# Kernel tuning notes

Measured on AMD Instinct MI355X. Metric: run time of the kernel, lower is better.

The kernel has to match this reference:

```python
import jax, jax.numpy as jnp
import numpy as np


def _phi(x):
    # ELU(x) + 1 feature map (positive kernel feature map)
    return jax.nn.elu(x) + 1.0


def setup_inputs() -> dict:
    key = jax.random.key(0)
    k1, k2, k3 = jax.random.split(key, 3)
    B, S, E = 4, 4096, 1024
    inputs = jax.random.normal(k1, (B, S, E), dtype=jnp.float32)
    mask = jnp.ones((B, S), dtype=jnp.float32)
    w_qkv = jax.random.normal(k2, (3 * E, E), dtype=jnp.float32) * (E ** -0.5)
    b_qkv = jax.random.normal(k3, (3 * E,), dtype=jnp.float32) * 0.02
    return {"inputs": inputs, "mask": mask, "w_qkv": w_qkv, "b_qkv": b_qkv, "num_heads": 16}


def reference(inputs, mask, w_qkv, b_qkv, num_heads):
    B, S, E = inputs.shape
    H = num_heads
    D = E // H
    # qkv projection: torch Linear is x @ W.T + b
    qkv = inputs @ w_qkv.T + b_qkv                     # (B, S, 3E)
    qkv = qkv.reshape(B, S, 3, H, D)
    q = qkv[:, :, 0]                                   # (B, S, H, D)
    k = qkv[:, :, 1]
    v = qkv[:, :, 2]
    # key masking (float multiply, as in einsum 'bshd,bs->bshd')
    k = k * mask[:, :, None, None]
    kq = _phi(q)                                       # (B, S, H, D)
    kk = _phi(k)                                       # (B, S, H, D)
    # kv outer-product accumulation over sequence: (B, H, M, D)
    kv = jnp.einsum('bshd,bshm->bhmd', kk, v)
    # normalizer
    z = 1.0 / (jnp.einsum('bshd,bhd->bsh', kq, kk.sum(axis=1)) + 1e-6)
    # final contraction
    attn = jnp.einsum('bshd,bhmd,bsh->bshm', kq, kv, z)  # (B, S, H, D)
    attn = attn.reshape(B, S, E)
    # NOTE: original forward computes a projection but returns `attn` (dropout is
    # identity at inference), so projection is dead code and omitted here.
    return attn
```

## Files before the change

### kernel.cpp

```cpp
#include <hip/hip_runtime.h>

typedef unsigned short u16;
typedef short bf16x8 __attribute__((ext_vector_type(8)));
typedef float f32x4 __attribute__((ext_vector_type(4)));
typedef u16 u16x8 __attribute__((ext_vector_type(8)));
typedef u16 u16x4 __attribute__((ext_vector_type(4)));

#define B_ 4
#define S_ 4096
#define E_ 1024
#define H_ 16
#define D_ 64
#define M_ 16384
#define N_ 3072
#define K_ 1024

__device__ __forceinline__ u16 f2b(float f) {
    unsigned x = __builtin_bit_cast(unsigned, f);
    return (u16)((x + 0x7fffu + ((x >> 16) & 1u)) >> 16);
}
__device__ __forceinline__ float b2f(u16 u) {
    unsigned x = ((unsigned)u) << 16;
    return __builtin_bit_cast(float, x);
}
__device__ __forceinline__ float phi_f(float x) { return x > 0.f ? x + 1.f : __expf(x); }

__device__ __forceinline__ void gload16(const void* g, void* l) {
    __builtin_amdgcn_global_load_lds((const __attribute__((address_space(1))) void*)g,
                                     (__attribute__((address_space(3))) void*)l, 16, 0, 0);
}

#define MEMFENCE asm volatile("" ::: "memory")
#define BAR { MEMFENCE; __builtin_amdgcn_s_barrier(); MEMFENCE; }
#define LGKM0 { asm volatile("s_waitcnt lgkmcnt(0)" ::: "memory"); \
                __builtin_amdgcn_sched_barrier(0); }
#define VMCNT(n) asm volatile("s_waitcnt vmcnt(" #n ")" ::: "memory")

__global__ void cvt_bf16(const float* __restrict__ in, u16* __restrict__ out, int n8) {
    int stride = gridDim.x * blockDim.x;
    for (int i = blockIdx.x * blockDim.x + threadIdx.x; i < n8; i += stride) {
        const float4* p = (const float4*)(in + (size_t)i * 8);
        float4 a = p[0], b = p[1];
        u16x8 o;
        o[0] = f2b(a.x); o[1] = f2b(a.y); o[2] = f2b(a.z); o[3] = f2b(a.w);
        o[4] = f2b(b.x); o[5] = f2b(b.y); o[6] = f2b(b.z); o[7] = f2b(b.w);
        *(u16x8*)(out + (size_t)i * 8) = o;
    }
}


#define RD_A(BO, MI0) { _Pragma("unroll") for (int m_ = 0; m_ < 4; ++m_) { \
    av[m_][0] = *(const bf16x8*)(aB + (BO) + (MI0 + m_) * 2048 + pc0); \
    av[m_][1] = *(const bf16x8*)(aB + (BO) + (MI0 + m_) * 2048 + pc1); } }

#define RD_B01(BO) { _Pragma("unroll") for (int n_ = 0; n_ < 2; ++n_) { \
    b01[n_][0] = *(const bf16x8*)(bB + (BO) + n_ * 2048 + pc0); \
    b01[n_][1] = *(const bf16x8*)(bB + (BO) + n_ * 2048 + pc1); } }

#define RD_B23(BO) { _Pragma("unroll") for (int n_ = 0; n_ < 2; ++n_) { \
    b23[n_][0] = *(const bf16x8*)(bB + (BO) + (2 + n_) * 2048 + pc0); \
    b23[n_][1] = *(const bf16x8*)(bB + (BO) + (2 + n_) * 2048 + pc1); } }

#define ST_A(TT, HI, BO) { \
    gload16(gA + (size_t)((HI) * 64) * K_ + (TT) * 64, lds + (BO) + (HI) * 8192 + t16); \
    gload16(gA + (size_t)((HI) * 64 + 128) * K_ + (TT) * 64, lds + (BO) + 16384 + (HI) * 8192 + t16); }

#define ST_B(TT, PR, BO) { \
    gload16(gB + (size_t)((PR) * 128) * K_ + (TT) * 64, lds + (BO) + 32768 + (PR) * 16384 + t16); \
    gload16(gB + (size_t)((PR) * 128 + 64) * K_ + (TT) * 64, lds + (BO) + 32768 + (PR) * 16384 + 8192 + t16); }

#define MM16(MI0, NI0, BV) { __builtin_amdgcn_s_setprio(1); \
    _Pragma("unroll") for (int m_ = 0; m_ < 4; ++m_) \
    _Pragma("unroll") for (int n_ = 0; n_ < 2; ++n_) \
    _Pragma("unroll") for (int h_ = 0; h_ < 2; ++h_) \
        acc[(MI0) + m_][(NI0) + n_] = __builtin_amdgcn_mfma_f32_16x16x32_bf16( \
            av[m_][h_], BV[n_][h_], acc[(MI0) + m_][(NI0) + n_], 0, 0, 0); \
    __builtin_amdgcn_s_setprio(0); }

__device__ __forceinline__ void run_tile(
    const u16* gA, const u16* gB, char* lds, int t16,
    const char* aB, const char* bB, int pc0, int pc1, f32x4 (&acc)[8][4])
{
    bf16x8 av[4][2], b01[2][2], b23[2][2];
    ST_A(0, 0, 0); ST_B(0, 0, 0); ST_B(0, 1, 0); ST_A(0, 1, 0);
    ST_A(1, 0, 65536); ST_B(1, 0, 65536);
    VMCNT(4);
    __builtin_amdgcn_s_barrier();
    MEMFENCE;
#pragma unroll 1
    for (int kt = 0; kt < 16; kt += 2) {
        int tp2 = kt + 2 < 16 ? kt + 2 : 15;
        int tp3 = kt + 3 < 16 ? kt + 3 : 15;
        RD_A(0, 0); RD_B01(0); ST_A(kt + 1, 1, 65536); BAR; LGKM0; MM16(0, 0, b01);
        RD_B23(0);  ST_B(kt + 1, 1, 65536);            BAR; LGKM0; MM16(0, 2, b23);
        RD_A(0, 4); ST_A(tp2, 0, 0);                   BAR; LGKM0; MM16(4, 2, b23);
        ST_B(tp2, 0, 0); VMCNT(4);                     BAR; LGKM0; MM16(4, 0, b01);
        RD_A(65536, 0); RD_B01(65536); ST_A(tp2, 1, 0); BAR; LGKM0; MM16(0, 0, b01);
        RD_B23(65536);  ST_B(tp2, 1, 0);                BAR; LGKM0; MM16(0, 2, b23);
        RD_A(65536, 4); ST_A(tp3, 0, 65536);            BAR; LGKM0; MM16(4, 2, b23);
        ST_B(tp3, 0, 65536); VMCNT(4);                  BAR; LGKM0; MM16(4, 0, b01);
    }
    VMCNT(0);
    __builtin_amdgcn_s_barrier();
    MEMFENCE;
}

__global__ __launch_bounds__(512, 2) void gemm_fused(
    const u16* __restrict__ Abf, const u16* __restrict__ Wbf,
    const float* __restrict__ bias, const float* __restrict__ mask,
    u16* __restrict__ KQ, u16* VT,
    float* __restrict__ KVP, float* __restrict__ KSP)
{
    __shared__ __align__(16) char lds[131072];

    int wg  = blockIdx.x;
    int xcd = wg & 7, ii = wg >> 3;
    int tm  = xcd * 8 + (ii >> 2);
    int g   = ii & 3;
    int m0  = tm << 8;
    int b   = tm >> 4;
    int s0  = (tm & 15) << 8;

    int t = threadIdx.x;
    int l = t & 63, wid = t >> 6;
    int wr = wid >> 2, wc = wid & 3;
    int lg = l >> 4, lr = l & 15;

    int srow  = t >> 3;
    int scolE = ((t & 7) ^ (srow & 7)) << 3;
    int t16   = t * 16;

    const u16* gA = Abf + (size_t)(m0 + srow) * K_ + scolE;
    const char* aB = lds + (wr * 128 + lr) * 128;
    const char* bB = lds + 32768 + (wc * 64 + lr) * 128;
    int pc0 = (lg * 16) ^ ((lr & 7) << 4);
    int pc1 = pc0 ^ 64;

    {
        int n0 = 2048 + g * 256;
        const u16* gB = Wbf + (size_t)(n0 + srow) * K_ + scolE;
        f32x4 acc[8][4] = {};
        run_tile(gA, gB, lds, t16, aB, bB, pc0, pc1, acc);
        float bv[4];
#pragma unroll
        for (int ni = 0; ni < 4; ++ni) bv[ni] = bias[n0 + wc * 64 + ni * 16 + lr];
        int h = g * 4 + wc;
#pragma unroll
        for (int mi = 0; mi < 8; ++mi) {
            int sbase = s0 + wr * 128 + mi * 16 + lg * 4;
#pragma unroll
            for (int ni = 0; ni < 4; ++ni) {
                u16x4 o;
#pragma unroll
                for (int j = 0; j < 4; ++j) o[j] = f2b(acc[mi][ni][j] + bv[ni]);
                int d = ni * 16 + lr;
                *(u16x4*)(VT + ((size_t)((b * H_ + h) * D_ + d)) * S_ + sbase) = o;
            }
        }
    }

    {
        int n0 = 1024 + g * 256;
        const u16* gB = Wbf + (size_t)(n0 + srow) * K_ + scolE;
        f32x4 acc[8][4] = {};
        run_tile(gA, gB, lds, t16, aB, bB, pc0, pc1, acc);
        float bv[4];
#pragma unroll
        for (int ni = 0; ni < 4; ++ni) bv[ni] = bias[n0 + wc * 64 + ni * 16 + lr];
#pragma unroll
        for (int mi = 0; mi < 8; ++mi) {
            int sl0 = wr * 128 + mi * 16 + lg * 4;
            float mk[4];
#pragma unroll
            for (int j = 0; j < 4; ++j) mk[j] = mask[m0 + sl0 + j];
#pragma unroll
            for (int ni = 0; ni < 4; ++ni) {
                int d = ni * 16 + lr;
                u16x4 o;
#pragma unroll
                for (int j = 0; j < 4; ++j)
                    o[j] = f2b(phi_f((acc[mi][ni][j] + bv[ni]) * mk[j]));
                *(u16x4*)(lds + wc * 32768 + d * 512 + ((sl0 * 2) ^ ((d & 7) << 4))) = o;
            }
        }
    }
    __syncthreads();

    {
        int head = wid & 3, mh = wid >> 2;
        int bh = b * 16 + g * 4 + head;
        f32x4 akv[2][4] = {};
        const u16* vbase = VT + ((size_t)(bh * 64 + mh * 32 + lr)) * S_ + s0;
#pragma unroll
        for (int ks = 0; ks < 8; ++ks) {
            bf16x8 vf[2];
#pragma unroll
            for (int mi = 0; mi < 2; ++mi)
                vf[mi] = *(const bf16x8*)(vbase + (size_t)mi * 16 * S_ + ks * 32 + lg * 8);
#pragma unroll
            for (int ni = 0; ni < 4; ++ni) {
                int dd = ni * 16 + lr;
                bf16x8 kf = *(const bf16x8*)(lds + head * 32768 + dd * 512 +
                                             ((ks * 64 + lg * 16) ^ ((dd & 7) << 4)));
                akv[0][ni] = __builtin_amdgcn_mfma_f32_16x16x32_bf16(vf[0], kf, akv[0][ni], 0, 0, 0);
                akv[1][ni] = __builtin_amdgcn_mfma_f32_16x16x32_bf16(vf[1], kf, akv[1][ni], 0, 0, 0);
            }
        }
        float* kvp = KVP + ((size_t)(tm & 15) * 64 + bh) * 4096;
#pragma unroll
        for (int mi = 0; mi < 2; ++mi)
#pragma unroll
            for (int ni = 0; ni < 4; ++ni)
#pragma unroll
                for (int j = 0; j < 4; ++j)
                    kvp[(mh * 32 + mi * 16 + lg * 4 + j) * 64 + ni * 16 + lr] = akv[mi][ni][j];
        int hd = t >> 7, dd2 = (t >> 1) & 63, hf = t & 1;
        float ksm = 0.f;
#pragma unroll
        for (int i = 0; i < 16; ++i) {
            bf16x8 kk8 = *(const bf16x8*)(lds + hd * 32768 + dd2 * 512 +
                                          ((hf * 256 + i * 16) ^ ((dd2 & 7) << 4)));
#pragma unroll
            for (int e = 0; e < 8; ++e) ksm += b2f((u16)kk8[e]);
        }
        ksm += __shfl_xor(ksm, 1);
        if (!hf) KSP[(tm & 15) * 4096 + (b * 16 + g * 4 + hd) * 64 + dd2] = ksm;
    }
    __syncthreads();

    {
        int n0 = g * 256;
        const u16* gB = Wbf + (size_t)(n0 + srow) * K_ + scolE;
        f32x4 acc[8][4] = {};
        run_tile(gA, gB, lds, t16, aB, bB, pc0, pc1, acc);
        float bv[4];
#pragma unroll
        for (int ni = 0; ni < 4; ++ni) bv[ni] = bias[n0 + wc * 64 + ni * 16 + lr];
#pragma unroll
        for (int mi = 0; mi < 8; ++mi)
#pragma unroll
            for (int j = 0; j < 4; ++j) {
                int row = m0 + wr * 128 + mi * 16 + lg * 4 + j;
#pragma unroll
                for (int ni = 0; ni < 4; ++ni) {
                    int col = n0 + wc * 64 + ni * 16 + lr;
                    KQ[(size_t)row * E_ + col] = f2b(phi_f(acc[mi][ni][j] + bv[ni]));
                }
            }
    }
}

__global__ void reduce_kv(const float* __restrict__ KVP, const float* __restrict__ KSP,
                          float* __restrict__ KV, float* __restrict__ KSUM)
{
    int g = blockIdx.x * 256 + threadIdx.x;
#pragma unroll 1
    for (int i = g * 4; i < g * 4 + 4; ++i) {
        float s = 0.f;
#pragma unroll
        for (int c = 0; c < 16; ++c) s += KVP[(size_t)c * (64 * 4096) + i];
        KV[i] = s;
    }
    if (g < 4096) {
        float s = 0.f;
#pragma unroll
        for (int c = 0; c < 16; ++c) s += KSP[c * 4096 + g];
        KSUM[g] = s;
    }
}

__global__ __launch_bounds__(256) void attn_out(
    const u16* __restrict__ KQ, const float* __restrict__ KV,
    const float* __restrict__ KSUM, float* __restrict__ Out)
{
    __shared__ __align__(16) u16 kqs[16384];
    __shared__ __align__(16) u16 bsm[5120];
    __shared__ float den[256];
    int bh = blockIdx.x, ch = blockIdx.y;
    int b = bh >> 4, h = bh & 15;
    int t = threadIdx.x;
    int l = t & 63, w = t >> 6;
    int lg = l >> 4, lr = l & 15;
    size_t row0 = (size_t)b * S_ + ch * 256;
    int srow = t >> 3, scol = (t & 7) << 3;
#pragma unroll
    for (int i = 0; i < 8; ++i)
        gload16(KQ + (row0 + srow + i * 32) * E_ + h * 64 + scol, kqs + i * 2048 + t * 8);

    const float* kvg = KV + bh * 4096;
#pragma unroll
    for (int ii = 0; ii < 16; ii += 4) {
        float4 v = *(const float4*)(kvg + t * 16 + ii);
        u16x4 o; o[0] = f2b(v.x); o[1] = f2b(v.y); o[2] = f2b(v.z); o[3] = f2b(v.w);
        *(u16x4*)&bsm[t * 16 + ii] = o;
    }
    if (t < 64) bsm[4096 + t] = f2b(KSUM[bh * 64 + t]);
    for (int i = t; i < 960; i += 256) bsm[4160 + i] = 0;
    __syncthreads();

    f32x4 acc[4][5] = {};
#pragma unroll
    for (int kh = 0; kh < 2; ++kh) {
        int ko = kh * 32 + lg * 8;
        bf16x8 af[4];
#pragma unroll
        for (int mi = 0; mi < 4; ++mi)
            af[mi] = *(const bf16x8*)&kqs[(w * 64 + mi * 16 + lr) * 64 + ko];
#pragma unroll
        for (int ni = 0; ni < 5; ++ni) {
            bf16x8 bb = *(const bf16x8*)&bsm[(ni * 16 + lr) * 64 + ko];
#pragma unroll
            for (int mi = 0; mi < 4; ++mi)
                acc[mi][ni] = __builtin_amdgcn_mfma_f32_16x16x32_bf16(af[mi], bb, acc[mi][ni], 0, 0, 0);
        }
    }
    if (lr == 0) {
#pragma unroll
        for (int mi = 0; mi < 4; ++mi)
#pragma unroll
            for (int j = 0; j < 4; ++j)
                den[w * 64 + mi * 16 + lg * 4 + j] = acc[mi][4][j];
    }
    __syncthreads();
#pragma unroll
    for (int mi = 0; mi < 4; ++mi)
#pragma unroll
        for (int j = 0; j < 4; ++j) {
            int sl = w * 64 + mi * 16 + lg * 4 + j;
            float z = 1.f / (den[sl] + 1e-6f);
            float* op = Out + (row0 + sl) * E_ + h * 64;
#pragma unroll
            for (int ni = 0; ni < 4; ++ni)
                op[ni * 16 + lr] = acc[mi][ni][j] * z;
        }
}

extern "C" void kernel_launch(void* const* d_in, const int* in_sizes, int n_in,
                              void* d_out, int out_size, void* d_ws, size_t ws_size,
                              hipStream_t stream)
{
    const float* inputs = (const float*)d_in[0];
    const float* mask   = (const float*)d_in[1];
    const float* w_qkv  = (const float*)d_in[2];
    const float* b_qkv  = (const float*)d_in[3];

    u16* Abf = (u16*)d_ws;
    u16* Wbf = Abf + (size_t)M_ * K_;
    u16* KQ  = Wbf + (size_t)N_ * K_;
    float* KVP  = (float*)(KQ + (size_t)M_ * E_);
    float* KSP  = KVP + 16 * 64 * 4096;
    float* KV   = KSP + 16 * 4096;
    float* KSUM = KV + 64 * 4096;

    u16* VT = (u16*)d_out;

    cvt_bf16<<<2048, 256, 0, stream>>>(inputs, Abf, M_ * K_ / 8);
    cvt_bf16<<<768, 256, 0, stream>>>(w_qkv, Wbf, N_ * K_ / 8);
    gemm_fused<<<256, 512, 0, stream>>>(Abf, Wbf, b_qkv, mask, KQ, VT, KVP, KSP);
    reduce_kv<<<256, 256, 0, stream>>>(KVP, KSP, KV, KSUM);
    attn_out<<<dim3(64, 16), 256, 0, stream>>>(KQ, KV, KSUM, (float*)d_out);
}
```

Measured before the change: 156.2 us.

## Split Q projection into a second GEMM fused with attention output

The Q-projection GEMM moves out of the V/K kernel into a new kernel that runs it after the KV reduction and applies phi(Q)·KV plus the normalizer straight from registers via LDS. This removes the bf16 KQ intermediate round-trip through HBM and the separate attn_out kernel. The reduction now emits a pre-swizzled bf16 KV/ksum block in one step. In exchange, the K/V GEMM kernel loses its overlap with the Q tile, and the new kernel adds an LDS staging phase and extra barriers after the main GEMM.

Measured after the change: 187.4 us. +20.0%, slower.

```diff
diff --git a/kernel.cpp b/kernel.cpp
--- a/kernel.cpp
+++ b/kernel.cpp
@@ -105,11 +105,10 @@
     MEMFENCE;
 }
 
-__global__ __launch_bounds__(512, 2) void gemm_fused(
+__global__ __launch_bounds__(512, 2) void gemm_vk(
     const u16* __restrict__ Abf, const u16* __restrict__ Wbf,
     const float* __restrict__ bias, const float* __restrict__ mask,
-    u16* __restrict__ KQ, u16* VT,
-    float* __restrict__ KVP, float* __restrict__ KSP)
+    u16* VT, float* __restrict__ KVP, float* __restrict__ KSP)
 {
     __shared__ __align__(16) char lds[131072];
 
@@ -226,113 +225,140 @@
         ksm += __shfl_xor(ksm, 1);
         if (!hf) KSP[(tm & 15) * 4096 + (b * 16 + g * 4 + hd) * 64 + dd2] = ksm;
     }
+}
+
+__global__ void reduce_kvb(const float* __restrict__ KVP, const float* __restrict__ KSP,
+                           u16* __restrict__ KVB)
+{
+    int bh = blockIdx.x;
+    int t = threadIdx.x;
+    int d = t & 63, mg = t >> 6;
+#pragma unroll 1
+    for (int i = 0; i < 16; ++i) {
+        int m = mg * 16 + i;
+        float s = 0.f;
+#pragma unroll
+        for (int c = 0; c < 16; ++c)
+            s += KVP[((size_t)c * 64 + bh) * 4096 + m * 64 + d];
+        KVB[((size_t)bh * 80 + m) * 64 + (d ^ ((m & 7) << 3))] = f2b(s);
+    }
+    if (mg == 0) {
+        float s = 0.f;
+#pragma unroll
+        for (int c = 0; c < 16; ++c) s += KSP[c * 4096 + bh * 64 + d];
+        KVB[((size_t)bh * 80 + 64) * 64 + d] = f2b(s);
+    }
+    for (int m = 65 + mg; m < 80; m += 4)
+        KVB[((size_t)bh * 80 + m) * 64 + (d ^ ((m & 7) << 3))] = 0;
+}
+
+__global__ __launch_bounds__(512, 2) void gemm_qattn(
+    const u16* __restrict__ Abf, const u16* __restrict__ Wbf,
+    const float* __restrict__ bias, const u16* __restrict__ KVB,
+    float* __restrict__ Out)
+{
+    __shared__ __align__(16) char lds[131072];
+
+    int wg  = blockIdx.x;
+    int xcd = wg & 7, ii = wg >> 3;
+    int tm  = xcd * 8 + (ii >> 2);
+    int g   = ii & 3;
+    int m0  = tm << 8;
+    int b   = tm >> 4;
+
+    int t = threadIdx.x;
+    int l = t & 63, wid = t >> 6;
+    int wr = wid >> 2, wc = wid & 3;
+    int lg = l >> 4, lr = l & 15;
+
+    int srow  = t >> 3;
+    int scolE = ((t & 7) ^ (srow & 7)) << 3;
+    int t16   = t * 16;
+
+    const u16* gA = Abf + (size_t)(m0 + srow) * K_ + scolE;
+    const char* aB = lds + (wr * 128 + lr) * 128;
+    const char* bB = lds + 32768 + (wc * 64 + lr) * 128;
+    int pc0 = (lg * 16) ^ ((lr & 7) << 4);
+    int pc1 = pc0 ^ 64;
+
+    int n0 = g * 256;
+    const u16* gB = Wbf + (size_t)(n0 + srow) * K_ + scolE;
+    f32x4 acc[8][4] = {};
+    run_tile(gA, gB, lds, t16, aB, bB, pc0, pc1, acc);
+
+    {
+        const u16* kvbg = KVB + (size_t)(b * 16 + g * 4) * 80 * 64;
+#pragma unroll
+        for (int i = 0; i < 5; ++i)
+            gload16(kvbg + i * 4096 + t * 8, lds + i * 8192 + t16);
+    }
+    float bv[4];
+#pragma unroll
+    for (int ni = 0; ni < 4; ++ni) bv[ni] = bias[n0 + wc * 64 + ni * 16 + lr];
+#pragma unroll
+    for (int mi = 0; mi < 8; ++mi)
+#pragma unroll
+        for (int ni = 0; ni < 4; ++ni)
+#pragma unroll
+            for (int j = 0; j < 4; ++j)
+                acc[mi][ni][j] = phi_f(acc[mi][ni][j] + bv[ni]);
+    VMCNT(0);
     __syncthreads();
 
-    {
-        int n0 = g * 256;
-        const u16* gB = Wbf + (size_t)(n0 + srow) * K_ + scolE;
-        f32x4 acc[8][4] = {};
-        run_tile(gA, gB, lds, t16, aB, bB, pc0, pc1, acc);
-        float bv[4];
-#pragma unroll
-        for (int ni = 0; ni < 4; ++ni) bv[ni] = bias[n0 + wc * 64 + ni * 16 + lr];
-#pragma unroll
-        for (int mi = 0; mi < 8; ++mi)
+#pragma unroll
+    for (int r = 0; r < 2; ++r) {
+        __syncthreads();
+        if (wr == r) {
+#pragma unroll
+            for (int mi = 0; mi < 8; ++mi)
+#pragma unroll
+                for (int j = 0; j < 4; ++j) {
+                    int sl = mi * 16 + lg * 4 + j;
+                    int swz = (sl & 7) << 4;
+#pragma unroll
+                    for (int ni = 0; ni < 4; ++ni) {
+                        int d2 = (ni * 16 + lr) * 2;
+                        *(u16*)(lds + 40960 + sl * 512 + wc * 128 + (d2 ^ swz)) =
+                            f2b(acc[mi][ni][j]);
+                    }
+                }
+        }
+        __syncthreads();
+
+        f32x4 a2[4][5] = {};
+#pragma unroll
+        for (int kh = 0; kh < 2; ++kh) {
+            bf16x8 af[4];
+#pragma unroll
+            for (int mi2 = 0; mi2 < 4; ++mi2) {
+                int sl = wr * 64 + mi2 * 16 + lr;
+                af[mi2] = *(const bf16x8*)(lds + 40960 + sl * 512 + wc * 128 +
+                                           ((kh * 64 + lg * 16) ^ ((sl & 7) << 4)));
+            }
+#pragma unroll
+            for (int ni2 = 0; ni2 < 5; ++ni2) {
+                int m = ni2 * 16 + lr;
+                bf16x8 bf_ = *(const bf16x8*)(lds + wc * 10240 + m * 128 +
+                                              ((kh * 64 + lg * 16) ^ ((m & 7) << 4)));
+#pragma unroll
+                for (int mi2 = 0; mi2 < 4; ++mi2)
+                    a2[mi2][ni2] = __builtin_amdgcn_mfma_f32_16x16x32_bf16(
+                        af[mi2], bf_, a2[mi2][ni2], 0, 0, 0);
+            }
+        }
+#pragma unroll
+        for (int mi2 = 0; mi2 < 4; ++mi2)
 #pragma unroll
             for (int j = 0; j < 4; ++j) {
-                int row = m0 + wr * 128 + mi * 16 + lg * 4 + j;
-#pragma unroll
-                for (int ni = 0; ni < 4; ++ni) {
-                    int col = n0 + wc * 64 + ni * 16 + lr;
-                    KQ[(size_t)row * E_ + col] = f2b(phi_f(acc[mi][ni][j] + bv[ni]));
-                }
-            }
-    }
-}
-
-__global__ void reduce_kv(const float* __restrict__ KVP, const float* __restrict__ KSP,
-                          float* __restrict__ KV, float* __restrict__ KSUM)
-{
-    int g = blockIdx.x * 256 + threadIdx.x;
-#pragma unroll 1
-    for (int i = g * 4; i < g * 4 + 4; ++i) {
-        float s = 0.f;
-#pragma unroll
-        for (int c = 0; c < 16; ++c) s += KVP[(size_t)c * (64 * 4096) + i];
-        KV[i] = s;
-    }
-    if (g < 4096) {
-        float s = 0.f;
-#pragma unroll
-        for (int c = 0; c < 16; ++c) s += KSP[c * 4096 + g];
-        KSUM[g] = s;
-    }
-}
-
-__global__ __launch_bounds__(256) void attn_out(
-    const u16* __restrict__ KQ, const float* __restrict__ KV,
-    const float* __restrict__ KSUM, float* __restrict__ Out)
-{
-    __shared__ __align__(16) u16 kqs[16384];
-    __shared__ __align__(16) u16 bsm[5120];
-    __shared__ float den[256];
-    int bh = blockIdx.x, ch = blockIdx.y;
-    int b = bh >> 4, h = bh & 15;
-    int t = threadIdx.x;
-    int l = t & 63, w = t >> 6;
-    int lg = l >> 4, lr = l & 15;
-    size_t row0 = (size_t)b * S_ + ch * 256;
-    int srow = t >> 3, scol = (t & 7) << 3;
-#pragma unroll
-    for (int i = 0; i < 8; ++i)
-        gload16(KQ + (row0 + srow + i * 32) * E_ + h * 64 + scol, kqs + i * 2048 + t * 8);
-
-    const float* kvg = KV + bh * 4096;
-#pragma unroll
-    for (int ii = 0; ii < 16; ii += 4) {
-        float4 v = *(const float4*)(kvg + t * 16 + ii);
-        u16x4 o; o[0] = f2b(v.x); o[1] = f2b(v.y); o[2] = f2b(v.z); o[3] = f2b(v.w);
-        *(u16x4*)&bsm[t * 16 + ii] = o;
-    }
-    if (t < 64) bsm[4096 + t] = f2b(KSUM[bh * 64 + t]);
-    for (int i = t; i < 960; i += 256) bsm[4160 + i] = 0;
-    __syncthreads();
-
-    f32x4 acc[4][5] = {};
-#pragma unroll
-    for (int kh = 0; kh < 2; ++kh) {
-        int ko = kh * 32 + lg * 8;
-        bf16x8 af[4];
-#pragma unroll
-        for (int mi = 0; mi < 4; ++mi)
-            af[mi] = *(const bf16x8*)&kqs[(w * 64 + mi * 16 + lr) * 64 + ko];
-#pragma unroll
-        for (int ni = 0; ni < 5; ++ni) {
-            bf16x8 bb = *(const bf16x8*)&bsm[(ni * 16 + lr) * 64 + ko];
-#pragma unroll
-            for (int mi = 0; mi < 4; ++mi)
-                acc[mi][ni] = __builtin_amdgcn_mfma_f32_16x16x32_bf16(af[mi], bb, acc[mi][ni], 0, 0, 0);
-        }
-    }
-    if (lr == 0) {
-#pragma unroll
-        for (int mi = 0; mi < 4; ++mi)
-#pragma unroll
-            for (int j = 0; j < 4; ++j)
-                den[w * 64 + mi * 16 + lg * 4 + j] = acc[mi][4][j];
-    }
-    __syncthreads();
-#pragma unroll
-    for (int mi = 0; mi < 4; ++mi)
-#pragma unroll
-        for (int j = 0; j < 4; ++j) {
-            int sl = w * 64 + mi * 16 + lg * 4 + j;
-            float z = 1.f / (den[sl] + 1e-6f);
-            float* op = Out + (row0 + sl) * E_ + h * 64;
-#pragma unroll
-            for (int ni = 0; ni < 4; ++ni)
-                op[ni * 16 + lr] = acc[mi][ni][j] * z;
-        }
+                float den = __shfl(a2[mi2][4][j], l & 48);
+                float z = 1.f / (den + 1e-6f);
+                int sg = (tm & 15) * 256 + r * 128 + wr * 64 + mi2 * 16 + lg * 4 + j;
+                float* op = Out + ((size_t)b * S_ + sg) * E_ + g * 256 + wc * 64;
+#pragma unroll
+                for (int ni2 = 0; ni2 < 4; ++ni2)
+                    op[ni2 * 16 + lr] = a2[mi2][ni2][j] * z;
+            }
+    }
 }
 
 extern "C" void kernel_launch(void* const* d_in, const int* in_sizes, int n_in,
@@ -346,17 +372,15 @@
 
     u16* Abf = (u16*)d_ws;
     u16* Wbf = Abf + (size_t)M_ * K_;
-    u16* KQ  = Wbf + (size_t)N_ * K_;
-    float* KVP  = (float*)(KQ + (size_t)M_ * E_);
-    float* KSP  = KVP + 16 * 64 * 4096;
-    float* KV   = KSP + 16 * 4096;
-    float* KSUM = KV + 64 * 4096;
+    float* KVP = (float*)(Wbf + (size_t)N_ * K_);
+    float* KSP = KVP + 16 * 64 * 4096;
+    u16* KVB   = (u16*)(KSP + 16 * 4096);
 
     u16* VT = (u16*)d_out;
 
     cvt_bf16<<<2048, 256, 0, stream>>>(inputs, Abf, M_ * K_ / 8);
     cvt_bf16<<<768, 256, 0, stream>>>(w_qkv, Wbf, N_ * K_ / 8);
-    gemm_fused<<<256, 512, 0, stream>>>(Abf, Wbf, b_qkv, mask, KQ, VT, KVP, KSP);
-    reduce_kv<<<256, 256, 0, stream>>>(KVP, KSP, KV, KSUM);
-    attn_out<<<dim3(64, 16), 256, 0, stream>>>(KQ, KV, KSUM, (float*)d_out);
-}
+    gemm_vk<<<256, 512, 0, stream>>>(Abf, Wbf, b_qkv, mask, VT, KVP, KSP);
+    reduce_kvb<<<64, 256, 0, stream>>>(KVP, KSP, KVB);
+    gemm_qattn<<<256, 512, 0, stream>>>(Abf, Wbf, b_qkv, KVB, (float*)d_out);
+}
```

## Double-buffer A fragments and overlap LDS reads with MFMA in GEMM loop

Applied to the files above, without the earlier changes.

The GEMM main loop now prefetches the next A/B register fragments from LDS before the current MFMA block, using two A fragment buffers and partial lgkmcnt waits instead of a full drain before each MFMA group. The MFMA order is rearranged so the register fragments in use rotate correctly. This is meant to hide LDS read latency behind matrix math. In exchange it needs more VGPRs, which could pressure the 2-waves-per-SIMD launch bound, and the hand-counted lgkmcnt values must exactly match the outstanding reads to stay correct.

Result: slower. 186.3 us (+19.3%).

```diff
diff --git a/kernel.cpp b/kernel.cpp
--- a/kernel.cpp
+++ b/kernel.cpp
@@ -32,9 +32,9 @@
 
 #define MEMFENCE asm volatile("" ::: "memory")
 #define BAR { MEMFENCE; __builtin_amdgcn_s_barrier(); MEMFENCE; }
-#define LGKM0 { asm volatile("s_waitcnt lgkmcnt(0)" ::: "memory"); \
-                __builtin_amdgcn_sched_barrier(0); }
 #define VMCNT(n) asm volatile("s_waitcnt vmcnt(" #n ")" ::: "memory")
+#define LGKM(n) asm volatile("s_waitcnt lgkmcnt(" #n ")" ::: "memory")
+#define SB0 __builtin_amdgcn_sched_barrier(0)
 
 __global__ void cvt_bf16(const float* __restrict__ in, u16* __restrict__ out, int n8) {
     int stride = gridDim.x * blockDim.x;
@@ -49,17 +49,13 @@
 }
 
 
-#define RD_A(BO, MI0) { _Pragma("unroll") for (int m_ = 0; m_ < 4; ++m_) { \
-    av[m_][0] = *(const bf16x8*)(aB + (BO) + (MI0 + m_) * 2048 + pc0); \
-    av[m_][1] = *(const bf16x8*)(aB + (BO) + (MI0 + m_) * 2048 + pc1); } }
-
-#define RD_B01(BO) { _Pragma("unroll") for (int n_ = 0; n_ < 2; ++n_) { \
-    b01[n_][0] = *(const bf16x8*)(bB + (BO) + n_ * 2048 + pc0); \
-    b01[n_][1] = *(const bf16x8*)(bB + (BO) + n_ * 2048 + pc1); } }
-
-#define RD_B23(BO) { _Pragma("unroll") for (int n_ = 0; n_ < 2; ++n_) { \
-    b23[n_][0] = *(const bf16x8*)(bB + (BO) + (2 + n_) * 2048 + pc0); \
-    b23[n_][1] = *(const bf16x8*)(bB + (BO) + (2 + n_) * 2048 + pc1); } }
+#define RD_A_TO(DST, BO, MI0) { _Pragma("unroll") for (int m_ = 0; m_ < 4; ++m_) { \
+    DST[m_][0] = *(const bf16x8*)(aB + (BO) + (MI0 + m_) * 2048 + pc0); \
+    DST[m_][1] = *(const bf16x8*)(aB + (BO) + (MI0 + m_) * 2048 + pc1); } }
+
+#define RD_B_TO(DST, BO, NI0) { _Pragma("unroll") for (int n_ = 0; n_ < 2; ++n_) { \
+    DST[n_][0] = *(const bf16x8*)(bB + (BO) + (NI0 + n_) * 2048 + pc0); \
+    DST[n_][1] = *(const bf16x8*)(bB + (BO) + (NI0 + n_) * 2048 + pc1); } }
 
 #define ST_A(TT, HI, BO) { \
     gload16(gA + (size_t)((HI) * 64) * K_ + (TT) * 64, lds + (BO) + (HI) * 8192 + t16); \
@@ -69,38 +65,48 @@
     gload16(gB + (size_t)((PR) * 128) * K_ + (TT) * 64, lds + (BO) + 32768 + (PR) * 16384 + t16); \
     gload16(gB + (size_t)((PR) * 128 + 64) * K_ + (TT) * 64, lds + (BO) + 32768 + (PR) * 16384 + 8192 + t16); }
 
-#define MM16(MI0, NI0, BV) { __builtin_amdgcn_s_setprio(1); \
+#define MM16(MI0, NI0, AV, BV) { __builtin_amdgcn_s_setprio(1); \
     _Pragma("unroll") for (int m_ = 0; m_ < 4; ++m_) \
     _Pragma("unroll") for (int n_ = 0; n_ < 2; ++n_) \
     _Pragma("unroll") for (int h_ = 0; h_ < 2; ++h_) \
         acc[(MI0) + m_][(NI0) + n_] = __builtin_amdgcn_mfma_f32_16x16x32_bf16( \
-            av[m_][h_], BV[n_][h_], acc[(MI0) + m_][(NI0) + n_], 0, 0, 0); \
+            AV[m_][h_], BV[n_][h_], acc[(MI0) + m_][(NI0) + n_], 0, 0, 0); \
     __builtin_amdgcn_s_setprio(0); }
 
 __device__ __forceinline__ void run_tile(
     const u16* gA, const u16* gB, char* lds, int t16,
     const char* aB, const char* bB, int pc0, int pc1, f32x4 (&acc)[8][4])
 {
-    bf16x8 av[4][2], b01[2][2], b23[2][2];
+    bf16x8 avX[4][2], avY[4][2], b01[2][2], b23[2][2];
     ST_A(0, 0, 0); ST_B(0, 0, 0); ST_B(0, 1, 0); ST_A(0, 1, 0);
     ST_A(1, 0, 65536); ST_B(1, 0, 65536);
     VMCNT(4);
     __builtin_amdgcn_s_barrier();
     MEMFENCE;
+    RD_A_TO(avX, 0, 0); RD_B_TO(b01, 0, 0);
 #pragma unroll 1
     for (int kt = 0; kt < 16; kt += 2) {
         int tp2 = kt + 2 < 16 ? kt + 2 : 15;
         int tp3 = kt + 3 < 16 ? kt + 3 : 15;
-        RD_A(0, 0); RD_B01(0); ST_A(kt + 1, 1, 65536); BAR; LGKM0; MM16(0, 0, b01);
-        RD_B23(0);  ST_B(kt + 1, 1, 65536);            BAR; LGKM0; MM16(0, 2, b23);
-        RD_A(0, 4); ST_A(tp2, 0, 0);                   BAR; LGKM0; MM16(4, 2, b23);
-        ST_B(tp2, 0, 0); VMCNT(4);                     BAR; LGKM0; MM16(4, 0, b01);
-        RD_A(65536, 0); RD_B01(65536); ST_A(tp2, 1, 0); BAR; LGKM0; MM16(0, 0, b01);
-        RD_B23(65536);  ST_B(tp2, 1, 0);                BAR; LGKM0; MM16(0, 2, b23);
-        RD_A(65536, 4); ST_A(tp3, 0, 65536);            BAR; LGKM0; MM16(4, 2, b23);
-        ST_B(tp3, 0, 65536); VMCNT(4);                  BAR; LGKM0; MM16(4, 0, b01);
+        ST_A(kt + 1, 1, 65536); BAR; RD_B_TO(b23, 0, 2);
+        LGKM(4); SB0; MM16(0, 0, avX, b01);
+        ST_B(kt + 1, 1, 65536); BAR; RD_A_TO(avY, 0, 4);
+        LGKM(8); SB0; MM16(0, 2, avX, b23);
+        ST_A(tp2, 0, 0); BAR;
+        LGKM(0); SB0; MM16(4, 2, avY, b23);
+        ST_B(tp2, 0, 0); VMCNT(4); BAR; RD_A_TO(avX, 65536, 0); RD_B_TO(b23, 65536, 2);
+        LGKM(12); SB0; MM16(4, 0, avY, b01);
+        ST_A(tp2, 1, 0); BAR; RD_B_TO(b01, 65536, 0);
+        LGKM(4); SB0; MM16(0, 2, avX, b23);
+        ST_B(tp2, 1, 0); BAR; RD_A_TO(avY, 65536, 4);
+        LGKM(8); SB0; MM16(0, 0, avX, b01);
+        ST_A(tp3, 0, 65536); BAR;
+        LGKM(0); SB0; MM16(4, 0, avY, b01);
+        ST_B(tp3, 0, 65536); VMCNT(4); BAR; RD_A_TO(avX, 0, 0); RD_B_TO(b01, 0, 0);
+        LGKM(12); SB0; MM16(4, 2, avY, b23);
     }
     VMCNT(0);
+    LGKM(0);
     __builtin_amdgcn_s_barrier();
     MEMFENCE;
 }
```
